# Optimization experiments

Hardware: AMD Instinct MI355X
Metric: run time of the kernel (lower is better)

Reference implementation:

```python
import jax, jax.numpy as jnp
import numpy as np

B, S, D, H = 2, 2048, 1024, 16
DK = D // H

def setup_inputs() -> dict:
    key = jax.random.key(0)
    ks = jax.random.split(key, 11)
    scale = 1.0 / np.sqrt(D)
    inp = {
        'q': jax.random.normal(ks[0], (B, S, D), jnp.float32),
        'k': jax.random.normal(ks[1], (B, S, D), jnp.float32),
        'v': jax.random.normal(ks[2], (B, S, D), jnp.float32),
        'Wq': jax.random.normal(ks[3], (D, D), jnp.float32) * scale,
        'bq': jnp.zeros((D,), jnp.float32),
        'Wk': jax.random.normal(ks[4], (D, D), jnp.float32) * scale,
        'bk': jnp.zeros((D,), jnp.float32),
        'Wv': jax.random.normal(ks[5], (D, D), jnp.float32) * scale,
        'bv': jnp.zeros((D,), jnp.float32),
        'Wo': jax.random.normal(ks[6], (D, D), jnp.float32) * scale,
        'bo': jnp.zeros((D,), jnp.float32),
    }
    return inp

def reference(q, k, v, Wq, bq, Wk, bk, Wv, bv, Wo, bo):
    # linear projections
    qp = q @ Wq + bq   # [B,S,D]
    kp = k @ Wk + bk
    vp = v @ Wv + bv
    # split heads -> [B,H,S,DK]
    qh = qp.reshape(B, S, H, DK).transpose(0, 2, 1, 3)
    kh = kp.reshape(B, S, H, DK).transpose(0, 2, 1, 3)
    vh = vp.reshape(B, S, H, DK).transpose(0, 2, 1, 3)
    scaled = jnp.einsum('bhqd,bhkd->bhqk', qh, kh) / jnp.sqrt(jnp.float32(DK))
    attn_score = jax.nn.softmax(scaled, axis=-1)  # [B,H,S,S]
    x = jnp.einsum('bhqk,bhkd->bhqd', attn_score, vh)
    # dropout is identity in eval mode
    out = x.transpose(0, 2, 1, 3).reshape(B, S, D)
    return (out @ Wo + bo, attn_score)
```

## Files before the change

kernel.cpp:

```cpp
#include <hip/hip_runtime.h>
#include <hip/hip_bf16.h>
#include <stdint.h>
#include <stddef.h>

typedef unsigned short u16;
typedef __attribute__((ext_vector_type(8))) short short8;
typedef __attribute__((ext_vector_type(4))) short bfx4;
typedef __attribute__((ext_vector_type(4))) float f32x4;
typedef __attribute__((ext_vector_type(4))) float f4;

constexpr int B_ = 2, S_ = 2048, D_ = 1024, H_ = 16;
constexpr size_t OUT_ELEMS = (size_t)B_ * S_ * D_;

__device__ __forceinline__ u16 f2bf(float f) {
    union { float f; unsigned u; } v; v.f = f;
    unsigned r = 0x7FFFu + ((v.u >> 16) & 1u);
    return (u16)((v.u + r) >> 16);
}

__device__ __forceinline__ unsigned cvtpk(float lo, float hi) {
    unsigned r;
    asm("v_cvt_pk_bf16_f32 %0, %1, %2" : "=v"(r) : "v"(lo), "v"(hi));
    return r;
}

__device__ __forceinline__ void gload16(const void* g, void* l) {
    auto gg = reinterpret_cast<const __attribute__((address_space(1))) unsigned*>(
        reinterpret_cast<uintptr_t>(g));
    auto ll = reinterpret_cast<__attribute__((address_space(3))) unsigned*>(
        reinterpret_cast<uintptr_t>(l));
    __builtin_amdgcn_global_load_lds(gg, ll, 16, 0, 0);
}

#define VMWAIT(N) do { asm volatile("s_waitcnt vmcnt(" #N ")" ::: "memory"); } while (0)
__device__ __forceinline__ void barrier_() {
    __builtin_amdgcn_s_barrier();
    __builtin_amdgcn_sched_barrier(0);
}

__global__ __launch_bounds__(256) void wtrans_kernel(
    const float* __restrict__ W0, const float* __restrict__ W1,
    const float* __restrict__ W2, const float* __restrict__ W3,
    u16* __restrict__ T0, u16* __restrict__ T1, u16* __restrict__ T2, u16* __restrict__ T3)
{
    __shared__ __align__(16) u16 Ts[64][72];
    const float* W = blockIdx.z == 0 ? W0 : blockIdx.z == 1 ? W1 : blockIdx.z == 2 ? W2 : W3;
    u16*         T = blockIdx.z == 0 ? T0 : blockIdx.z == 1 ? T1 : blockIdx.z == 2 ? T2 : T3;
    const int t = threadIdx.x;
    const int r0 = blockIdx.y * 64, c0 = blockIdx.x * 64;
    const int row = t >> 2, qd = t & 3;

    const float* src = W + (size_t)(r0 + row) * 1024 + c0 + qd * 16;
    u16 tmp[16];
    #pragma unroll
    for (int j = 0; j < 16; j += 4) {
        f4 v = *(const f4*)(src + j);
        tmp[j] = f2bf(v[0]); tmp[j+1] = f2bf(v[1]); tmp[j+2] = f2bf(v[2]); tmp[j+3] = f2bf(v[3]);
    }
    #pragma unroll
    for (int j = 0; j < 16; j++) Ts[row][qd * 16 + j] = tmp[j];
    __syncthreads();
    short8 o0, o1;
    #pragma unroll
    for (int j = 0; j < 8; j++) { o0[j] = (short)Ts[qd*16 + j][row]; o1[j] = (short)Ts[qd*16 + 8 + j][row]; }
    u16* dst = T + (size_t)(c0 + row) * 1024 + r0 + qd * 16;
    *(short8*)dst = o0;
    *(short8*)(dst + 8) = o1;
}

struct Stage { short8 h[2]; };

__device__ __forceinline__ void stage_load_f32(Stage& st, const float* Af, int row0, int K, int k0, int t) {
    const int row = t >> 1, half = t & 1;
    const float* p = Af + (size_t)(row0 + row) * K + k0 + half * 16;
    #pragma unroll
    for (int j = 0; j < 2; j++) {
        f4 v0 = *(const f4*)(p + j * 8);
        f4 v1 = *(const f4*)(p + j * 8 + 4);
        short8 hh;
        hh[0]=(short)f2bf(v0[0]); hh[1]=(short)f2bf(v0[1]); hh[2]=(short)f2bf(v0[2]); hh[3]=(short)f2bf(v0[3]);
        hh[4]=(short)f2bf(v1[0]); hh[5]=(short)f2bf(v1[1]); hh[6]=(short)f2bf(v1[2]); hh[7]=(short)f2bf(v1[3]);
        st.h[j] = hh;
    }
}

__device__ __forceinline__ void stage_store_f32(const Stage& st, u16* Ls, int t) {
    const int row = t >> 1, half = t & 1;
    #pragma unroll
    for (int j = 0; j < 2; j++) {
        int byteo = half * 32 + j * 16;
        *(short8*)((char*)Ls + row * 64 + (byteo ^ ((row & 3) << 4))) = st.h[j];
    }
}

__global__ __launch_bounds__(256, 3)
void gemm_qkv(const float* __restrict__ A0, const float* __restrict__ A1, const float* __restrict__ A2,
              const u16* __restrict__ Bt0, const u16* __restrict__ Bt1, const u16* __restrict__ Bt2,
              const float* __restrict__ bi0, const float* __restrict__ bi1, const float* __restrict__ bi2,
              u16* __restrict__ Cq, u16* __restrict__ Ck, u16* __restrict__ Vt)
{
    constexpr int K = D_, N = D_;
    __shared__ __align__(16) u16 As[2][128 * 32];
    __shared__ __align__(16) u16 Bs[2][128 * 32];

    const int z = blockIdx.z;
    const float* Aptr = z == 0 ? A0  : z == 1 ? A1  : A2;
    const u16*   Bt   = z == 0 ? Bt0 : z == 1 ? Bt1 : Bt2;
    const float* bias = z == 0 ? bi0 : z == 1 ? bi1 : bi2;

    const int t = threadIdx.x;
    const int w = t >> 6, l = t & 63, lr = l >> 4, lc = l & 15;
    const int wr = w >> 1, wc = w & 1;
    const int id = blockIdx.y * 8 + blockIdx.x;
    const int xcd = id & 7, i_ = id >> 3;
    const int row0 = ((xcd << 2) | ((i_ >> 4) << 1) | ((i_ >> 3) & 1)) * 128;
    const int col0 = (i_ & 7) * 128;
    const int NI = K >> 5;

    auto issueB = [&](int i, u16* dst) {
        #pragma unroll
        for (int j = 0; j < 2; j++) {
            int off = j * 256 + t;
            int row = off >> 2, ch = off & 3;
            const char* src = (const char*)Bt + (((size_t)(col0 + row) * K + i * 32) << 1)
                              + ((ch ^ (row & 3)) << 4);
            gload16(src, (char*)dst + off * 16);
        }
    };

    f32x4 acc[4][4] = {};
    Stage sa;
    issueB(0, Bs[0]);
    stage_load_f32(sa, Aptr, row0, K, 0, t);

    for (int i = 0; i < NI; i++) {
        const int p = i & 1;
        stage_store_f32(sa, As[p], t);
        __syncthreads();
        if (i + 1 < NI) {
            issueB(i + 1, Bs[p ^ 1]);
            stage_load_f32(sa, Aptr, row0, K, (i + 1) * 32, t);
        }

        short8 af[4], bf_[4];
        #pragma unroll
        for (int mm = 0; mm < 4; mm++) {
            int r = wr * 64 + mm * 16 + lc;
            af[mm] = *(const short8*)((const char*)As[p] + r * 64 + ((lr * 16) ^ ((r & 3) << 4)));
        }
        #pragma unroll
        for (int nn = 0; nn < 4; nn++) {
            int r = wc * 64 + nn * 16 + lc;
            bf_[nn] = *(const short8*)((const char*)Bs[p] + r * 64 + ((lr * 16) ^ ((r & 3) << 4)));
        }
        #pragma unroll
        for (int mm = 0; mm < 4; mm++)
            #pragma unroll
            for (int nn = 0; nn < 4; nn++)
                acc[mm][nn] = __builtin_amdgcn_mfma_f32_16x16x32_bf16(af[mm], bf_[nn], acc[mm][nn], 0, 0, 0);
        __builtin_amdgcn_s_barrier();
    }

    float bv[4];
    #pragma unroll
    for (int nn = 0; nn < 4; nn++) bv[nn] = bias[col0 + wc * 64 + nn * 16 + lc];

    if (z == 2) {
        #pragma unroll
        for (int mm = 0; mm < 4; mm++) {
            const int row = row0 + wr * 64 + mm * 16 + lr * 4;
            const int b = row >> 11, s = row & 2047;
            #pragma unroll
            for (int nn = 0; nn < 4; nn++) {
                const int col = col0 + wc * 64 + nn * 16 + lc;
                const int h = col >> 6, d = col & 63;
                bfx4 o;
                #pragma unroll
                for (int r = 0; r < 4; r++) o[r] = (short)f2bf(acc[mm][nn][r] + bv[nn]);
                *(bfx4*)(Vt + (((size_t)((b * 16 + h) * 64 + d)) << 11) + s) = o;
            }
        }
    } else {
        u16* Cptr = z == 0 ? Cq : Ck;
        const float scale = z == 0 ? 0.125f : 1.0f;
        #pragma unroll
        for (int mm = 0; mm < 4; mm++) {
            const int row = row0 + wr * 64 + mm * 16 + lr * 4;
            #pragma unroll
            for (int nn = 0; nn < 4; nn++) {
                const int col = col0 + wc * 64 + nn * 16 + lc;
                #pragma unroll
                for (int r = 0; r < 4; r++)
                    Cptr[(size_t)(row + r) * N + col] = f2bf((acc[mm][nn][r] + bv[nn]) * scale);
            }
        }
    }
}

__global__ __launch_bounds__(256, 3)
void gemm_out(const u16* __restrict__ Aptr, const u16* __restrict__ Bt,
              const float* __restrict__ bias, float* __restrict__ Cptr)
{
    constexpr int K = D_, N = D_;
    __shared__ __align__(16) u16 As[2][128 * 32];
    __shared__ __align__(16) u16 Bs[2][128 * 32];

    const int t = threadIdx.x;
    const int w = t >> 6, l = t & 63, lr = l >> 4, lc = l & 15;
    const int wr = w >> 1, wc = w & 1;
    const int id = blockIdx.y * 8 + blockIdx.x;
    const int xcd = id & 7, i_ = id >> 3;
    const int row0 = ((xcd << 2) | ((i_ >> 4) << 1) | ((i_ >> 3) & 1)) * 128;
    const int col0 = (i_ & 7) * 128;
    const int NI = K >> 5;

    auto issueT = [&](const u16* P, int r0_, int i, u16* dst) {
        #pragma unroll
        for (int j = 0; j < 2; j++) {
            int off = j * 256 + t;
            int row = off >> 2, ch = off & 3;
            const char* src = (const char*)P + (((size_t)(r0_ + row) * K + i * 32) << 1)
                              + ((ch ^ (row & 3)) << 4);
            gload16(src, (char*)dst + off * 16);
        }
    };

    f32x4 acc[4][4] = {};
    issueT(Bt, col0, 0, Bs[0]);
    issueT(Aptr, row0, 0, As[0]);

    for (int i = 0; i < NI; i++) {
        const int p = i & 1;
        if (i + 1 < NI) {
            issueT(Bt, col0, i + 1, Bs[p ^ 1]);
            issueT(Aptr, row0, i + 1, As[p ^ 1]);
            VMWAIT(4);
        } else {
            VMWAIT(0);
        }
        barrier_();

        short8 af[4], bf_[4];
        #pragma unroll
        for (int mm = 0; mm < 4; mm++) {
            int r = wr * 64 + mm * 16 + lc;
            af[mm] = *(const short8*)((const char*)As[p] + r * 64 + ((lr * 16) ^ ((r & 3) << 4)));
        }
        #pragma unroll
        for (int nn = 0; nn < 4; nn++) {
            int r = wc * 64 + nn * 16 + lc;
            bf_[nn] = *(const short8*)((const char*)Bs[p] + r * 64 + ((lr * 16) ^ ((r & 3) << 4)));
        }
        #pragma unroll
        for (int mm = 0; mm < 4; mm++)
            #pragma unroll
            for (int nn = 0; nn < 4; nn++)
                acc[mm][nn] = __builtin_amdgcn_mfma_f32_16x16x32_bf16(af[mm], bf_[nn], acc[mm][nn], 0, 0, 0);
        __builtin_amdgcn_s_barrier();
    }

    float bv[4];
    #pragma unroll
    for (int nn = 0; nn < 4; nn++) bv[nn] = bias[col0 + wc * 64 + nn * 16 + lc];

    #pragma unroll
    for (int mm = 0; mm < 4; mm++) {
        const int row = row0 + wr * 64 + mm * 16 + lr * 4;
        #pragma unroll
        for (int nn = 0; nn < 4; nn++) {
            const int col = col0 + wc * 64 + nn * 16 + lc;
            #pragma unroll
            for (int r = 0; r < 4; r++)
                Cptr[(size_t)(row + r) * N + col] = acc[mm][nn][r] + bv[nn];
        }
    }
}

__global__ __launch_bounds__(512, 4)
void attn_kernel(const u16* __restrict__ qp, const u16* __restrict__ kp,
                 const u16* __restrict__ vt, float* __restrict__ Pout,
                 u16* __restrict__ xout)
{
    __shared__ __align__(16) u16 Qs[128 * 64];
    __shared__ __align__(16) u16 Ks[2][128 * 64];
    __shared__ __align__(16) u16 Vts[2][64 * 128];

    const int t = threadIdx.x;
    const int w = t >> 6, l = t & 63, lr = l >> 4, lc = l & 15;
    const int bid = blockIdx.x;
    const int s = ((bid & 7) << 6) | (bid >> 3);
    const int q0 = (s & 15) * 128;
    const int bh = s >> 4, b = bh >> 4, h = bh & 15;
    const float L2E = 1.4426950408889634f;
    constexpr int NT = S_ / 128;

    auto issueK = [&](int kt, int buf) {
        #pragma unroll
        for (int i = 0; i < 2; i++) {
            int off = i * 512 + t, row = off >> 3, ch = off & 7;
            const char* src = (const char*)kp + ((((size_t)b * S_ + kt * 128 + row) * D_ + h * 64) << 1)
                              + ((ch ^ (row & 7)) << 4);
            gload16(src, (char*)Ks[buf] + off * 16);
        }
    };
    auto issueV = [&](int kt, int buf) {
        #pragma unroll
        for (int i = 0; i < 2; i++) {
            int off = i * 512 + t, row = off >> 4, ch = off & 15;
            const char* src = (const char*)vt + ((((size_t)bh * 64 + row) * S_ + kt * 128) << 1)
                              + ((ch ^ (row & 7)) << 4);
            gload16(src, (char*)Vts[buf] + off * 16);
        }
    };

    issueK(0, 0);
    #pragma unroll
    for (int i = 0; i < 2; i++) {
        int c = t + 512 * i, row = c >> 3, ch = c & 7;
        short8 vq = *(const short8*)(qp + ((size_t)b * S_ + q0 + row) * D_ + h * 64 + ch * 8);
        *(short8*)((char*)Qs + row * 128 + ((ch * 16) ^ ((row & 7) << 4))) = vq;
    }
    __syncthreads();

    short8 qf[2];
    {
        int r = w * 16 + lc, sw = (r & 7) << 4;
        const char* qb = (const char*)Qs + r * 128;
        qf[0] = *(const short8*)(qb + ((lr * 16) ^ sw));
        qf[1] = *(const short8*)(qb + ((64 + lr * 16) ^ sw));
    }

    float sum = 0.f;
    for (int kt = 0; kt < NT; kt++) {
        const int p = kt & 1;
        if (kt + 1 < NT) { issueK(kt + 1, p ^ 1); VMWAIT(2); }
        else             { VMWAIT(0); }
        barrier_();
        const char* Kb = (const char*)Ks[p];
        #pragma unroll
        for (int f = 0; f < 8; f++) {
            int r = f * 16 + lc, sw = (r & 7) << 4;
            const char* kb = Kb + r * 128;
            short8 k0 = *(const short8*)(kb + ((lr * 16) ^ sw));
            short8 k1 = *(const short8*)(kb + ((64 + lr * 16) ^ sw));
            f32x4 sacc = {};
            sacc = __builtin_amdgcn_mfma_f32_16x16x32_bf16(k0, qf[0], sacc, 0, 0, 0);
            sacc = __builtin_amdgcn_mfma_f32_16x16x32_bf16(k1, qf[1], sacc, 0, 0, 0);
            sum += exp2f(sacc[0] * L2E) + exp2f(sacc[1] * L2E)
                 + exp2f(sacc[2] * L2E) + exp2f(sacc[3] * L2E);
        }
        __builtin_amdgcn_s_barrier();
    }
    issueK(0, 0); issueV(0, 0);
    sum += __shfl_xor(sum, 16);
    sum += __shfl_xor(sum, 32);
    const float inv = 1.0f / sum;

    f32x4 xacc[4] = {};
    float* pbase = Pout + ((size_t)bh * S_ + q0 + w * 16 + lc) * S_ + lr * 4;

    for (int kt = 0; kt < NT; kt++) {
        const int p = kt & 1;
        if (kt + 1 < NT) { issueK(kt + 1, p ^ 1); issueV(kt + 1, p ^ 1); }
        if (kt == 0)           VMWAIT(4);
        else if (kt + 1 < NT)  VMWAIT(12);
        else                   VMWAIT(8);
        barrier_();
        const char* Kb = (const char*)Ks[p];
        const char* Vb = (const char*)Vts[p];

        #pragma unroll
        for (int kk = 0; kk < 4; kk++) {
            union { unsigned u[4]; short8 s8; } pu;
            #pragma unroll
            for (int fo = 0; fo < 2; fo++) {
                const int f = kk * 2 + fo;
                int r = f * 16 + lc, sw = (r & 7) << 4;
                const char* kb = Kb + r * 128;
                short8 k0 = *(const short8*)(kb + ((lr * 16) ^ sw));
                short8 k1 = *(const short8*)(kb + ((64 + lr * 16) ^ sw));
                f32x4 sacc = {};
                __builtin_amdgcn_s_setprio(1);
                sacc = __builtin_amdgcn_mfma_f32_16x16x32_bf16(k0, qf[0], sacc, 0, 0, 0);
                sacc = __builtin_amdgcn_mfma_f32_16x16x32_bf16(k1, qf[1], sacc, 0, 0, 0);
                __builtin_amdgcn_s_setprio(0);
                f32x4 pv_;
                pv_[0] = exp2f(sacc[0] * L2E) * inv;
                pv_[1] = exp2f(sacc[1] * L2E) * inv;
                pv_[2] = exp2f(sacc[2] * L2E) * inv;
                pv_[3] = exp2f(sacc[3] * L2E) * inv;
                *(f32x4*)(pbase + (size_t)kt * 128 + f * 16) = pv_;
                pu.u[fo * 2 + 0] = cvtpk(pv_[0], pv_[1]);
                pu.u[fo * 2 + 1] = cvtpk(pv_[2], pv_[3]);
            }
            const short8 pa = pu.s8;
            __builtin_amdgcn_s_setprio(1);
            #pragma unroll
            for (int n = 0; n < 4; n++) {
                int rr = n * 16 + lc, sw2 = (rr & 7) << 4;
                const char* vrow = Vb + rr * 256;
                union { bfx4 h[2]; short8 s8; } vu;
                vu.h[0] = *(const bfx4*)(vrow + ((kk * 64 + lr * 8) ^ sw2));
                vu.h[1] = *(const bfx4*)(vrow + ((kk * 64 + 32 + lr * 8) ^ sw2));
                xacc[n] = __builtin_amdgcn_mfma_f32_16x16x32_bf16(pa, vu.s8, xacc[n], 0, 0, 0);
            }
            __builtin_amdgcn_s_setprio(0);
        }
        __builtin_amdgcn_s_barrier();
    }

    #pragma unroll
    for (int n = 0; n < 4; n++) {
        #pragma unroll
        for (int r = 0; r < 4; r++) {
            int row = q0 + w * 16 + lr * 4 + r;
            int col = h * 64 + n * 16 + lc;
            xout[((size_t)b * S_ + row) * D_ + col] = f2bf(xacc[n][r]);
        }
    }
}

extern "C" void kernel_launch(void* const* d_in, const int* in_sizes, int n_in,
                              void* d_out, int out_size, void* d_ws, size_t ws_size,
                              hipStream_t stream)
{
    const float* qin = (const float*)d_in[0];
    const float* kin = (const float*)d_in[1];
    const float* vin = (const float*)d_in[2];
    const float* Wq  = (const float*)d_in[3];
    const float* bq  = (const float*)d_in[4];
    const float* Wk  = (const float*)d_in[5];
    const float* bk  = (const float*)d_in[6];
    const float* Wv  = (const float*)d_in[7];
    const float* bv  = (const float*)d_in[8];
    const float* Wo  = (const float*)d_in[9];
    const float* bo  = (const float*)d_in[10];

    u16* base = (u16*)d_ws;
    u16* Wqt = base;
    u16* Wkt = base + 1048576;
    u16* Wvt = base + 2097152;
    u16* Wot = base + 3145728;
    u16* qpb = base + 4194304;
    u16* kpb = base + 8388608;
    u16* vtb = base + 12582912;
    u16* xb  = base + 16777216;

    float* out  = (float*)d_out;
    float* Pout = out + OUT_ELEMS;

    wtrans_kernel<<<dim3(16, 16, 4), 256, 0, stream>>>(Wq, Wk, Wv, Wo, Wqt, Wkt, Wvt, Wot);
    gemm_qkv<<<dim3(8, 32, 3), 256, 0, stream>>>(
        qin, kin, vin, Wqt, Wkt, Wvt, bq, bk, bv, qpb, kpb, vtb);
    attn_kernel<<<512, 512, 0, stream>>>(qpb, kpb, vtb, Pout, xb);
    gemm_out<<<dim3(8, 32), 256, 0, stream>>>(xb, Wot, bo, out);
}
```

Baseline: 281.1 us.

## Move V transpose out of QKV GEMM epilogue into separate kernel; fold softmax normalization into exp

```diff
diff --git a/kernel.cpp b/kernel.cpp
--- a/kernel.cpp
+++ b/kernel.cpp
@@ -66,6 +66,29 @@
     u16* dst = T + (size_t)(c0 + row) * 1024 + r0 + qd * 16;
     *(short8*)dst = o0;
     *(short8*)(dst + 8) = o1;
+}
+
+__global__ __launch_bounds__(256) void vtrans_kernel(const u16* __restrict__ vp, u16* __restrict__ vt)
+{
+    __shared__ __align__(16) u16 Vs[64][72];
+    const int t = threadIdx.x;
+    const int s0 = blockIdx.x * 64;
+    const int bh = blockIdx.y, b = bh >> 4, h = bh & 15;
+    #pragma unroll
+    for (int i = 0; i < 2; i++) {
+        int c = t + 256 * i, row = c >> 3, ch = c & 7;
+        *(short8*)(&Vs[row][ch * 8]) =
+            *(const short8*)(vp + ((size_t)b * S_ + s0 + row) * D_ + h * 64 + ch * 8);
+    }
+    __syncthreads();
+    #pragma unroll
+    for (int i = 0; i < 2; i++) {
+        int c = t + 256 * i, d = c >> 3, ch = c & 7;
+        short8 o;
+        #pragma unroll
+        for (int j = 0; j < 8; j++) o[j] = (short)Vs[ch * 8 + j][d];
+        *(short8*)(vt + ((size_t)bh * 64 + d) * S_ + s0 + ch * 8) = o;
+    }
 }
 
 struct Stage { short8 h[2]; };
@@ -97,7 +120,7 @@
 void gemm_qkv(const float* __restrict__ A0, const float* __restrict__ A1, const float* __restrict__ A2,
               const u16* __restrict__ Bt0, const u16* __restrict__ Bt1, const u16* __restrict__ Bt2,
               const float* __restrict__ bi0, const float* __restrict__ bi1, const float* __restrict__ bi2,
-              u16* __restrict__ Cq, u16* __restrict__ Ck, u16* __restrict__ Vt)
+              u16* __restrict__ Cq, u16* __restrict__ Ck, u16* __restrict__ Cv)
 {
     constexpr int K = D_, N = D_;
     __shared__ __align__(16) u16 As[2][128 * 32];
@@ -107,6 +130,8 @@
     const float* Aptr = z == 0 ? A0  : z == 1 ? A1  : A2;
     const u16*   Bt   = z == 0 ? Bt0 : z == 1 ? Bt1 : Bt2;
     const float* bias = z == 0 ? bi0 : z == 1 ? bi1 : bi2;
+    u16*         Cptr = z == 0 ? Cq  : z == 1 ? Ck  : Cv;
+    const float scale = z == 0 ? 0.125f : 1.0f;
 
     const int t = threadIdx.x;
     const int w = t >> 6, l = t & 63, lr = l >> 4, lc = l & 15;
@@ -165,34 +190,15 @@
     #pragma unroll
     for (int nn = 0; nn < 4; nn++) bv[nn] = bias[col0 + wc * 64 + nn * 16 + lc];
 
-    if (z == 2) {
-        #pragma unroll
-        for (int mm = 0; mm < 4; mm++) {
-            const int row = row0 + wr * 64 + mm * 16 + lr * 4;
-            const int b = row >> 11, s = row & 2047;
-            #pragma unroll
-            for (int nn = 0; nn < 4; nn++) {
-                const int col = col0 + wc * 64 + nn * 16 + lc;
-                const int h = col >> 6, d = col & 63;
-                bfx4 o;
-                #pragma unroll
-                for (int r = 0; r < 4; r++) o[r] = (short)f2bf(acc[mm][nn][r] + bv[nn]);
-                *(bfx4*)(Vt + (((size_t)((b * 16 + h) * 64 + d)) << 11) + s) = o;
-            }
-        }
-    } else {
-        u16* Cptr = z == 0 ? Cq : Ck;
-        const float scale = z == 0 ? 0.125f : 1.0f;
-        #pragma unroll
-        for (int mm = 0; mm < 4; mm++) {
-            const int row = row0 + wr * 64 + mm * 16 + lr * 4;
-            #pragma unroll
-            for (int nn = 0; nn < 4; nn++) {
-                const int col = col0 + wc * 64 + nn * 16 + lc;
-                #pragma unroll
-                for (int r = 0; r < 4; r++)
-                    Cptr[(size_t)(row + r) * N + col] = f2bf((acc[mm][nn][r] + bv[nn]) * scale);
-            }
+    #pragma unroll
+    for (int mm = 0; mm < 4; mm++) {
+        const int row = row0 + wr * 64 + mm * 16 + lr * 4;
+        #pragma unroll
+        for (int nn = 0; nn < 4; nn++) {
+            const int col = col0 + wc * 64 + nn * 16 + lc;
+            #pragma unroll
+            for (int r = 0; r < 4; r++)
+                Cptr[(size_t)(row + r) * N + col] = f2bf((acc[mm][nn][r] + bv[nn]) * scale);
         }
     }
 }
@@ -354,7 +360,7 @@
     issueK(0, 0); issueV(0, 0);
     sum += __shfl_xor(sum, 16);
     sum += __shfl_xor(sum, 32);
-    const float inv = 1.0f / sum;
+    const float l2i = -log2f(sum);
 
     f32x4 xacc[4] = {};
     float* pbase = Pout + ((size_t)bh * S_ + q0 + w * 16 + lc) * S_ + lr * 4;
@@ -385,10 +391,10 @@
                 sacc = __builtin_amdgcn_mfma_f32_16x16x32_bf16(k1, qf[1], sacc, 0, 0, 0);
                 __builtin_amdgcn_s_setprio(0);
                 f32x4 pv_;
-                pv_[0] = exp2f(sacc[0] * L2E) * inv;
-                pv_[1] = exp2f(sacc[1] * L2E) * inv;
-                pv_[2] = exp2f(sacc[2] * L2E) * inv;
-                pv_[3] = exp2f(sacc[3] * L2E) * inv;
+                pv_[0] = exp2f(fmaf(sacc[0], L2E, l2i));
+                pv_[1] = exp2f(fmaf(sacc[1], L2E, l2i));
+                pv_[2] = exp2f(fmaf(sacc[2], L2E, l2i));
+                pv_[3] = exp2f(fmaf(sacc[3], L2E, l2i));
                 *(f32x4*)(pbase + (size_t)kt * 128 + f * 16) = pv_;
                 pu.u[fo * 2 + 0] = cvtpk(pv_[0], pv_[1]);
                 pu.u[fo * 2 + 1] = cvtpk(pv_[2], pv_[3]);
@@ -443,15 +449,17 @@
     u16* Wot = base + 3145728;
     u16* qpb = base + 4194304;
     u16* kpb = base + 8388608;
-    u16* vtb = base + 12582912;
-    u16* xb  = base + 16777216;
+    u16* vpb = base + 12582912;
+    u16* vtb = base + 16777216;
+    u16* xb  = base + 20971520;
 
     float* out  = (float*)d_out;
     float* Pout = out + OUT_ELEMS;
 
     wtrans_kernel<<<dim3(16, 16, 4), 256, 0, stream>>>(Wq, Wk, Wv, Wo, Wqt, Wkt, Wvt, Wot);
     gemm_qkv<<<dim3(8, 32, 3), 256, 0, stream>>>(
-        qin, kin, vin, Wqt, Wkt, Wvt, bq, bk, bv, qpb, kpb, vtb);
+        qin, kin, vin, Wqt, Wkt, Wvt, bq, bk, bv, qpb, kpb, vpb);
+    vtrans_kernel<<<dim3(32, 32), 256, 0, stream>>>(vpb, vtb);
     attn_kernel<<<512, 512, 0, stream>>>(qpb, kpb, vtb, Pout, xb);
     gemm_out<<<dim3(8, 32), 256, 0, stream>>>(xb, Wot, bo, out);
 }
```

New measurement: 285.3 us. No clear change (+1.5%).
